# Optimization experiments

Measured on AMD Instinct MI355X. Metric: run time of the kernel, lower is better.

## Reference

```python
import jax, jax.numpy as jnp
import numpy as np

B, N, H, L, K, R = 1024, 64, 128, 4, 16, 20
CUTOFF = 5.0
GAMMA = 10.0   # RBF width
N_TYPES = 10

def _rn(k, shape, scale):
    return jax.random.normal(k, shape, jnp.float32) * scale

def setup_inputs():
    key = jax.random.key(0)
    ks = jax.random.split(key, 16)
    z = lambda *s: jnp.zeros(s, jnp.float32)
    return {
        "positions": _rn(ks[0], (B, N, 3), 2.0),
        "atomic_numbers": jax.random.randint(ks[1], (B, N), 0, N_TYPES),
        "atom_embed": _rn(ks[2], (N_TYPES, H // 4), 0.1),
        "pos_W": _rn(ks[3], (3, 3 * H // 4), 0.5),
        "pos_b": z(3 * H // 4),
        "msg_W": _rn(ks[4], (L, 2 * H + R, H), (2 * H + R) ** -0.5),
        "msg_b": z(L, H),
        "upd_W": _rn(ks[5], (L, H, H), H ** -0.5),
        "upd_b": z(L, H),
        "gself_W": _rn(ks[6], (L, H, H), H ** -0.5),
        "gmean_W": _rn(ks[7], (L, H, H), H ** -0.5),
        "g_b": z(L, H),
        "fus_W": _rn(ks[8], (L, 2 * H, H), (2 * H) ** -0.5),
        "fus_b": z(L, H),
        "ln_g": jnp.ones((L, H), jnp.float32),
        "ln_b": z(L, H),
        "cb_W1": _rn(ks[9], (L, H, 4 * H), H ** -0.5),
        "cb_b1": z(L, 4 * H),
        "cb_W2": _rn(ks[10], (L, 4 * H, H), (4 * H) ** -0.5),
        "cb_b2": z(L, H),
        "fo_W1": _rn(ks[11], (H, H), H ** -0.5),
        "fo_b1": z(H),
        "fo_W2": _rn(ks[12], (H, 3), H ** -0.5),
        "fo_b2": z(3),
    }

def _ln(x, g, b):
    m = x.mean(-1, keepdims=True)
    v = ((x - m) ** 2).mean(-1, keepdims=True)
    return (x - m) * jax.lax.rsqrt(v + 1e-5) * g + b

def reference(positions, atomic_numbers, atom_embed, pos_W, pos_b, msg_W, msg_b,
              upd_W, upd_b, gself_W, gmean_W, g_b, fus_W, fus_b, ln_g, ln_b,
              cb_W1, cb_b1, cb_W2, cb_b2, fo_W1, fo_b1, fo_W2, fo_b2):
    silu = jax.nn.silu
    Bb, Nn, _ = positions.shape
    # embeddings: atom type (H/4) || position (3H/4)
    h = jnp.concatenate([atom_embed[atomic_numbers], positions @ pos_W + pos_b], -1)  # [B,N,H]
    # kNN graph from positions (static across layers since positions are fixed)
    diff = positions[:, :, None, :] - positions[:, None, :, :]
    d2 = jnp.sum(diff * diff, -1) + jnp.eye(Nn, dtype=positions.dtype) * 1e9  # exclude self
    neg_d2, idx = jax.lax.top_k(-d2, K)                       # [B,N,K]
    d = jnp.sqrt(jnp.maximum(-neg_d2, 1e-12))
    centers = jnp.linspace(0.0, CUTOFF, R).astype(positions.dtype)
    rbf = jnp.exp(-GAMMA * (d[..., None] - centers) ** 2)     # [B,N,K,R]
    env = (0.5 * (jnp.cos(jnp.pi * d / CUTOFF) + 1.0) * (d < CUTOFF))[..., None]  # cosine cutoff
    idx_flat = idx.reshape(Bb, Nn * K)
    for i in range(msg_W.shape[0]):
        # local MPNN: gather neighbors, message MLP on [h_i, h_j, rbf], envelope, sum
        h_j = jnp.take_along_axis(h, idx_flat[:, :, None], axis=1).reshape(Bb, Nn, K, -1)
        h_i = jnp.broadcast_to(h[:, :, None, :], h_j.shape)
        m = silu(jnp.concatenate([h_i, h_j, rbf], -1) @ msg_W[i] + msg_b[i]) * env
        local = h + silu(m.sum(2) @ upd_W[i] + upd_b[i])
        # Clifford mean-field: self transform + global-mean transform
        glob = silu(h @ gself_W[i] + h.mean(1, keepdims=True) @ gmean_W[i] + g_b[i])
        # fusion (dropout is identity at inference)
        fused = silu(jnp.concatenate([local, glob], -1) @ fus_W[i] + fus_b[i])
        # Clifford block: pre-LN residual MLP
        x = _ln(fused, ln_g[i], ln_b[i])
        h = fused + silu(x @ cb_W1[i] + cb_b1[i]) @ cb_W2[i] + cb_b2[i]
    return silu(h @ fo_W1 + fo_b1) @ fo_W2 + fo_b2  # [B,N,3] forces
```

## Files before the change

kernel.cpp:

```cpp
#include <hip/hip_runtime.h>

typedef unsigned short ushort_t;
typedef unsigned int uint_t;
typedef unsigned long long ull_t;
typedef __attribute__((ext_vector_type(8))) short short8;
typedef __attribute__((ext_vector_type(4))) float f32x4;

#define B_ 1024
#define N_ 64
#define H_ 128
#define NT 256

#define IMG_WI 0
#define IMG_WJ 16384
#define IMG_UW 32768
#define IMG_GS 49152
#define IMG_FT 65536
#define IMG_FB 81920
#define IMG_C1 98304
#define IMG_C2 163840
#define IMG_GMT 229376
#define IMG_RW 245760
#define IMG_L 249856
#define IMG_FO 999424
#define WS_WEIGHTS (2u*1024u*1024u)
#define KNN_STRIDE 12288u

__device__ __forceinline__ ushort_t f2bf(float f) {
    uint_t u = __float_as_uint(f);
    return (ushort_t)((u + 0x7fffu + ((u >> 16) & 1u)) >> 16);
}
__device__ __forceinline__ float bf2f(ushort_t u) {
    union { uint_t i; float f; } v; v.i = ((uint_t)u) << 16; return v.f;
}
__device__ __forceinline__ float siluf(float x) { return x / (1.0f + __expf(-x)); }

__device__ __forceinline__ int sidx(int m, int k) {
    return m * H_ + (((k >> 3) ^ (m & 7)) << 3) + (k & 7);
}
__device__ __forceinline__ int fragoff(int m, int ch) {
    return m * H_ + ((ch ^ (m & 7)) << 3);
}

extern "C" __global__ __launch_bounds__(256)
void convert_weights(const float* __restrict__ msg_W, const float* __restrict__ upd_W,
                     const float* __restrict__ gself_W, const float* __restrict__ fus_W,
                     const float* __restrict__ cb_W1, const float* __restrict__ cb_W2,
                     const float* __restrict__ gmean_W, const float* __restrict__ fo_W1,
                     ushort_t* __restrict__ wimg)
{
    const int g = blockIdx.x;
    if (g >= 244) {
        int st = g - 244;
        ushort_t* dst = wimg + IMG_FO + st * 4096;
        for (int e = 0; e < 16; ++e) {
            int q = threadIdx.x * 16 + e;
            int n = q >> 7, k = q & 127;
            dst[q] = f2bf(fo_W1[(size_t)k * 128 + st * 32 + n]);
        }
        return;
    }
    const int l = g / 61, r = g - l * 61;
    ushort_t* base = wimg + l * IMG_L;
    if (r == 60) {
        const float* W = msg_W + l * 35328 + 256 * 128;
        ushort_t* dst = base + IMG_RW;
        for (int e = 0; e < 16; ++e) {
            int q = threadIdx.x * 16 + e;
            int sub = q >> 10, n = (q >> 5) & 31, k = q & 31;
            dst[q] = f2bf(k < 20 ? W[(size_t)k * 128 + sub * 32 + n] : 0.0f);
        }
        return;
    }
    const float* W; int ld = 128, k0 = 0, c0, off, st;
    if      (r < 4)  { W = msg_W + l * 35328;            st = r;      off = IMG_WI;  c0 = st * 32; }
    else if (r < 8)  { W = msg_W + l * 35328;  k0 = 128; st = r - 4;  off = IMG_WJ;  c0 = st * 32; }
    else if (r < 12) { W = upd_W + l * 16384;            st = r - 8;  off = IMG_UW;  c0 = st * 32; }
    else if (r < 16) { W = gself_W + l * 16384;          st = r - 12; off = IMG_GS;  c0 = st * 32; }
    else if (r < 20) { W = fus_W + l * 32768;            st = r - 16; off = IMG_FT;  c0 = st * 32; }
    else if (r < 24) { W = fus_W + l * 32768;  k0 = 128; st = r - 20; off = IMG_FB;  c0 = st * 32; }
    else if (r < 40) { W = cb_W1 + l * 65536;  ld = 512; st = r - 24; off = IMG_C1;  c0 = st * 32; }
    else if (r < 56) { int j = (r - 40) >> 2; W = cb_W2 + l * 65536; k0 = j * 128;
                       st = r - 40; off = IMG_C2; c0 = ((r - 40) & 3) * 32; }
    else             { W = gmean_W + l * 16384;          st = r - 56; off = IMG_GMT; c0 = st * 32; }
    ushort_t* dst = base + off + st * 4096;
    for (int e = 0; e < 16; ++e) {
        int q = threadIdx.x * 16 + e;
        int n = q >> 7, k = q & 127;
        dst[q] = f2bf(W[(size_t)(k0 + k) * ld + c0 + n]);
    }
}

extern "C" __global__ __launch_bounds__(64)
void knn_kernel(const float* __restrict__ positions, char* __restrict__ ws)
{
    const int b = blockIdx.x, lane = threadIdx.x;
    float px = positions[b * 192 + lane * 3 + 0];
    float py = positions[b * 192 + lane * 3 + 1];
    float pz = positions[b * 192 + lane * 3 + 2];
    float* kd = (float*)(ws + WS_WEIGHTS + (size_t)b * KNN_STRIDE);
    float* ke = kd + 1024;
    ushort_t* ki = (ushort_t*)(ke + 1024);
    for (int n = 0; n < 64; ++n) {
        float dx = __fsub_rn(__shfl(px, n), px);
        float dy = __fsub_rn(__shfl(py, n), py);
        float dz = __fsub_rn(__shfl(pz, n), pz);
        float d2 = __fadd_rn(__fadd_rn(__fmul_rn(dx, dx), __fmul_rn(dy, dy)), __fmul_rn(dz, dz));
        if (lane == n) d2 = 1e30f;
        float sd = 0.f; int si = 0;
        for (int k = 0; k < 16; ++k) {
            float dmin = d2;
            #pragma unroll
            for (int o = 1; o < 64; o <<= 1) dmin = fminf(dmin, __shfl_xor(dmin, o));
            ull_t mask = __ballot(d2 == dmin);
            int widx = __ffsll(mask) - 1;
            if (lane == widx) d2 = 1e30f;
            if (lane == k) { si = widx; sd = dmin; }
        }
        if (lane < 16) {
            float dd = sqrtf(fmaxf(sd, 1e-12f));
            kd[n * 16 + lane] = dd;
            ke[n * 16 + lane] = (dd < 5.0f) ? 0.5f * (__cosf(0.62831853071795864769f * dd) + 1.0f) : 0.0f;
            ki[n * 16 + lane] = (ushort_t)si;
        }
    }
}

#define HFS 132
struct __align__(16) Smem {
    ushort_t T1[N_ * H_];
    ushort_t T2[N_ * H_];
    float Hf[N_ * HFS];
    float d[1024];
    float env[1024];
    ushort_t idx[1024];
    char u[2048];
};

__device__ __forceinline__ f32x4 gemm_s(const short8 a[4], const ushort_t* __restrict__ img,
                                        int s, int l15, int quad)
{
    const ushort_t* base = img + ((s >> 1) << 12) + ((((s & 1) << 4) + l15) << 7) + quad * 8;
    short8 b0 = *(const short8*)(base);
    short8 b1 = *(const short8*)(base + 32);
    short8 b2 = *(const short8*)(base + 64);
    short8 b3 = *(const short8*)(base + 96);
    f32x4 c = {0.f, 0.f, 0.f, 0.f};
    c = __builtin_amdgcn_mfma_f32_16x16x32_bf16(a[0], b0, c, 0, 0, 0);
    c = __builtin_amdgcn_mfma_f32_16x16x32_bf16(a[1], b1, c, 0, 0, 0);
    c = __builtin_amdgcn_mfma_f32_16x16x32_bf16(a[2], b2, c, 0, 0, 0);
    c = __builtin_amdgcn_mfma_f32_16x16x32_bf16(a[3], b3, c, 0, 0, 0);
    return c;
}
__device__ __forceinline__ f32x4 gemm_s_acc(const short8 a[4], const ushort_t* __restrict__ img,
                                            int s, int l15, int quad, f32x4 c)
{
    const ushort_t* base = img + ((s >> 1) << 12) + ((((s & 1) << 4) + l15) << 7) + quad * 8;
    short8 b0 = *(const short8*)(base);
    short8 b1 = *(const short8*)(base + 32);
    short8 b2 = *(const short8*)(base + 64);
    short8 b3 = *(const short8*)(base + 96);
    c = __builtin_amdgcn_mfma_f32_16x16x32_bf16(a[0], b0, c, 0, 0, 0);
    c = __builtin_amdgcn_mfma_f32_16x16x32_bf16(a[1], b1, c, 0, 0, 0);
    c = __builtin_amdgcn_mfma_f32_16x16x32_bf16(a[2], b2, c, 0, 0, 0);
    c = __builtin_amdgcn_mfma_f32_16x16x32_bf16(a[3], b3, c, 0, 0, 0);
    return c;
}
__device__ __forceinline__ void loadA(const ushort_t* __restrict__ X, int mrow, int quad, short8 a[4]) {
    #pragma unroll
    for (int kc = 0; kc < 4; ++kc) a[kc] = *(const short8*)&X[fragoff(mrow, kc * 4 + quad)];
}
__device__ __forceinline__ void buildA(const float* __restrict__ Hf, int mrow, int quad, short8 a[4]) {
    #pragma unroll
    for (int kc = 0; kc < 4; ++kc) {
        const float* p = Hf + mrow * HFS + (kc * 4 + quad) * 8;
        float4 u0 = *(const float4*)p;
        float4 u1 = *(const float4*)(p + 4);
        short8 v;
        v[0] = (short)f2bf(u0.x); v[1] = (short)f2bf(u0.y);
        v[2] = (short)f2bf(u0.z); v[3] = (short)f2bf(u0.w);
        v[4] = (short)f2bf(u1.x); v[5] = (short)f2bf(u1.y);
        v[6] = (short)f2bf(u1.z); v[7] = (short)f2bf(u1.w);
        a[kc] = v;
    }
}

extern "C" __global__ __launch_bounds__(NT, 2)
void md17_fused_kernel(
    const float* __restrict__ positions, const int* __restrict__ atomic_numbers,
    const float* __restrict__ atom_embed, const float* __restrict__ pos_W,
    const float* __restrict__ pos_b,
    const float* __restrict__ msg_b, const float* __restrict__ upd_b,
    const float* __restrict__ g_b, const float* __restrict__ fus_b,
    const float* __restrict__ ln_g, const float* __restrict__ ln_b,
    const float* __restrict__ cb_b1, const float* __restrict__ cb_b2,
    const float* __restrict__ fo_b1,
    const float* __restrict__ fo_W2, const float* __restrict__ fo_b2,
    char* __restrict__ ws, float* __restrict__ out)
{
    __shared__ Smem sm;
    const int b = blockIdx.x;
    const int tid = threadIdx.x;
    const int wave = tid >> 6, lane = tid & 63;
    const int quad = lane >> 4, l15 = lane & 15;
    const int mrow = wave * 16 + l15;
    const int rbase = wave * 16 + quad * 4;

    const ushort_t* wimg = (const ushort_t*)ws;
    float* spos = (float*)sm.u;
    ushort_t* part = (ushort_t*)sm.u;
    float* hmean = (float*)(sm.u + 1024);
    float* gvec  = (float*)(sm.u + 1536);

    {
        const char* kb = ws + WS_WEIGHTS + (size_t)b * KNN_STRIDE;
        const float* kd = (const float*)kb;
        const float* ke = (const float*)(kb + 4096);
        const uint_t* ki = (const uint_t*)(kb + 8192);
        for (int t = tid; t < 1024; t += NT) { sm.d[t] = kd[t]; sm.env[t] = ke[t]; }
        for (int t = tid; t < 512; t += NT) ((uint_t*)sm.idx)[t] = ki[t];
        if (tid < 192) spos[tid] = positions[b * 192 + tid];
    }
    __syncthreads();
    for (int t = tid; t < N_ * H_; t += NT) {
        int n = t >> 7, f = t & 127;
        float v;
        if (f < 32) {
            v = atom_embed[atomic_numbers[b * N_ + n] * 32 + f];
        } else {
            int j = f - 32;
            v = pos_b[j];
            #pragma unroll
            for (int c = 0; c < 3; ++c)
                v = fmaf(spos[n * 3 + c], pos_W[c * 96 + j], v);
        }
        sm.Hf[n * HFS + f] = v;
        sm.T1[sidx(n, f)] = f2bf(v);
    }
    __syncthreads();

    #pragma unroll 1
    for (int l = 0; l < 4; ++l) {
        const ushort_t* wl = wimg + l * IMG_L;
        const float* mb  = msg_b + l * H_;
        const float* ub  = upd_b + l * H_;
        const float* gb  = g_b + l * H_;
        const float* fb  = fus_b + l * H_;
        const float* lg  = ln_g + l * H_;
        const float* lb  = ln_b + l * H_;
        const float* c1b = cb_b1 + l * 4 * H_;
        const float* c2b = cb_b2 + l * H_;

        #pragma unroll
        for (int s = 0; s < 8; ++s) {
            int col = s * 16 + l15;
            const float* hp = sm.Hf + rbase * HFS + col;
            float p = hp[0] + hp[HFS] + hp[2 * HFS] + hp[3 * HFS];
            p += __shfl_xor(p, 16);
            p += __shfl_xor(p, 32);
            if (quad == 0) part[wave * 128 + col] = f2bf(p);
        }
        __syncthreads();
        if (tid < H_)
            hmean[tid] = (bf2f(part[tid]) + bf2f(part[128 + tid])
                        + bf2f(part[256 + tid]) + bf2f(part[384 + tid])) * (1.0f / 64.0f);
        __syncthreads();

        if (tid < H_) {
            float s = gb[tid];
            const ushort_t* wrow = wl + IMG_GMT + tid * 128;
            for (int c = 0; c < 128; c += 8) {
                short8 w = *(const short8*)(wrow + c);
                #pragma unroll
                for (int i = 0; i < 8; ++i) s = fmaf(hmean[c + i], bf2f((ushort_t)w[i]), s);
            }
            gvec[tid] = s;
        }
        {
            short8 a_h[4]; loadA(sm.T1, mrow, quad, a_h);
            #pragma unroll
            for (int s = 0; s < 8; ++s) {
                f32x4 c = gemm_s(a_h, wl + IMG_WI, s, l15, quad);
                int col = s * 16 + l15; float bv = mb[col];
                #pragma unroll
                for (int r = 0; r < 4; ++r)
                    sm.T1[sidx(rbase + r, col)] = f2bf(c[r] + bv);
            }
            #pragma unroll
            for (int s = 0; s < 8; ++s) {
                f32x4 c = gemm_s(a_h, wl + IMG_WJ, s, l15, quad);
                int col = s * 16 + l15;
                #pragma unroll
                for (int r = 0; r < 4; ++r)
                    sm.T2[sidx(rbase + r, col)] = f2bf(c[r]);
            }
        }
        __syncthreads();

        {
            float ccv[8];
            #pragma unroll
            for (int j = 0; j < 8; ++j)
                ccv[j] = (float)((double)(quad * 8 + j) * (5.0 / 19.0));
            #pragma unroll 1
            for (int g = 0; g < 16; ++g) {
                int n = wave * 16 + g;
                int jv[4]; float ev[4];
                #pragma unroll
                for (int r = 0; r < 4; ++r) {
                    int k = quad * 4 + r;
                    jv[r] = sm.idx[n * 16 + k];
                    ev[r] = sm.env[n * 16 + k];
                }
                float ddm = sm.d[n * 16 + l15];
                short8 arb;
                #pragma unroll
                for (int j = 0; j < 8; ++j) {
                    float t2 = ddm - ccv[j];
                    float rv = __expf(-10.0f * t2 * t2);
                    arb[j] = (short)((quad * 8 + j) < 20 ? f2bf(rv) : (ushort_t)0);
                }
                #pragma unroll
                for (int s = 0; s < 8; ++s) {
                    int col = s * 16 + l15;
                    const ushort_t* rbase_p = wl + IMG_RW + ((s >> 1) << 10)
                                            + ((((s & 1) << 4) + l15) << 5) + quad * 8;
                    short8 brw = *(const short8*)rbase_p;
                    f32x4 c = {0.f, 0.f, 0.f, 0.f};
                    c = __builtin_amdgcn_mfma_f32_16x16x32_bf16(arb, brw, c, 0, 0, 0);
                    float ai = bf2f(sm.T1[sidx(n, col)]);
                    float acc = 0.f;
                    #pragma unroll
                    for (int r = 0; r < 4; ++r) {
                        float gm = bf2f(sm.T2[sidx(jv[r], col)]);
                        acc = fmaf(siluf(ai + gm + c[r]), ev[r], acc);
                    }
                    acc += __shfl_xor(acc, 16);
                    acc += __shfl_xor(acc, 32);
                    if (quad == 0) sm.T1[sidx(n, col)] = f2bf(acc);
                }
            }
        }
        __syncthreads();


        {
            short8 a_m[4]; loadA(sm.T1, mrow, quad, a_m);
            #pragma unroll
            for (int s = 0; s < 8; ++s) {
                f32x4 c = gemm_s(a_m, wl + IMG_UW, s, l15, quad);
                int col = s * 16 + l15; float bv = ub[col];
                #pragma unroll
                for (int r = 0; r < 4; ++r)
                    sm.T2[sidx(rbase + r, col)] = f2bf(sm.Hf[(rbase + r) * HFS + col] + siluf(c[r] + bv));
            }
            short8 a_hh[4]; buildA(sm.Hf, mrow, quad, a_hh);
            #pragma unroll
            for (int s = 0; s < 8; ++s) {
                f32x4 c = gemm_s(a_hh, wl + IMG_GS, s, l15, quad);
                int col = s * 16 + l15; float gv = gvec[col];
                #pragma unroll
                for (int r = 0; r < 4; ++r)
                    sm.T1[sidx(rbase + r, col)] = f2bf(siluf(c[r] + gv));
            }
        }

        float sr[4] = {0.f, 0.f, 0.f, 0.f}, qr[4] = {0.f, 0.f, 0.f, 0.f};
        {
            short8 a_t[4];
            loadA(sm.T2, mrow, quad, a_t);
            #pragma unroll
            for (int s = 0; s < 8; ++s) {
                f32x4 c = gemm_s(a_t, wl + IMG_FT, s, l15, quad);
                int col = s * 16 + l15;
                int rb = rbase * HFS + col;
                sm.Hf[rb] = c[0]; sm.Hf[rb + HFS] = c[1];
                sm.Hf[rb + 2 * HFS] = c[2]; sm.Hf[rb + 3 * HFS] = c[3];
            }
            loadA(sm.T1, mrow, quad, a_t);
            #pragma unroll
            for (int s = 0; s < 8; ++s) {
                f32x4 c = gemm_s(a_t, wl + IMG_FB, s, l15, quad);
                int col = s * 16 + l15; float bv = fb[col];
                int rb = rbase * HFS + col;
                #pragma unroll
                for (int r = 0; r < 4; ++r) {
                    float v = siluf(sm.Hf[rb + r * HFS] + c[r] + bv);
                    sm.Hf[rb + r * HFS] = v;
                    sr[r] += v; qr[r] += v * v;
                }
            }
            #pragma unroll
            for (int o = 1; o < 16; o <<= 1) {
                #pragma unroll
                for (int r = 0; r < 4; ++r) {
                    sr[r] += __shfl_xor(sr[r], o);
                    qr[r] += __shfl_xor(qr[r], o);
                }
            }
        }

        #pragma unroll
        for (int r = 0; r < 4; ++r) {
            float mu = sr[r] * (1.0f / 128.0f);
            float var = qr[r] * (1.0f / 128.0f) - mu * mu;
            float rs = rsqrtf(var + 1e-5f);
            int row = rbase + r;
            #pragma unroll
            for (int s = 0; s < 8; ++s) {
                int col = s * 16 + l15;
                sm.T1[sidx(row, col)] = f2bf((sm.Hf[row * HFS + col] - mu) * rs * lg[col] + lb[col]);
            }
        }

        {
            short8 a_x[4]; loadA(sm.T1, mrow, quad, a_x);
            f32x4 acc2[8];
            #pragma unroll
            for (int s = 0; s < 8; ++s) acc2[s] = (f32x4){0.f, 0.f, 0.f, 0.f};
            #pragma unroll 1
            for (int j = 0; j < 4; ++j) {
                #pragma unroll
                for (int s = 0; s < 8; ++s) {
                    f32x4 c = gemm_s(a_x, wl + IMG_C1 + j * 16384, s, l15, quad);
                    int col = s * 16 + l15; float bv = c1b[j * H_ + col];
                    #pragma unroll
                    for (int r = 0; r < 4; ++r)
                        sm.T2[sidx(rbase + r, col)] = f2bf(siluf(c[r] + bv));
                }
                short8 a_t[4]; loadA(sm.T2, mrow, quad, a_t);
                #pragma unroll
                for (int s = 0; s < 8; ++s)
                    acc2[s] = gemm_s_acc(a_t, wl + IMG_C2 + j * 16384, s, l15, quad, acc2[s]);
            }
            #pragma unroll
            for (int s = 0; s < 8; ++s) {
                int col = s * 16 + l15; float bv = c2b[col];
                #pragma unroll
                for (int r = 0; r < 4; ++r) {
                    int row = rbase + r;
                    float v = sm.Hf[row * HFS + col] + acc2[s][r] + bv;
                    sm.Hf[row * HFS + col] = v;
                    sm.T1[sidx(row, col)] = f2bf(v);
                }
            }
        }
    }

    {
        short8 a_f[4]; loadA(sm.T1, mrow, quad, a_f);
        #pragma unroll
        for (int s = 0; s < 8; ++s) {
            f32x4 c = gemm_s(a_f, wimg + IMG_FO, s, l15, quad);
            int col = s * 16 + l15; float bv = fo_b1[col];
            #pragma unroll
            for (int r = 0; r < 4; ++r)
                sm.T2[sidx(rbase + r, col)] = f2bf(siluf(c[r] + bv));
        }
    }
    __syncthreads();
    if (tid < 192) {
        int n = tid / 3, j = tid - n * 3;
        float s = fo_b2[j];
        for (int c = 0; c < H_; ++c)
            s = fmaf(bf2f(sm.T2[sidx(n, c)]), fo_W2[c * 3 + j], s);
        out[b * 192 + tid] = s;
    }
}

extern "C" void kernel_launch(void* const* d_in, const int* in_sizes, int n_in,
                              void* d_out, int out_size, void* d_ws, size_t ws_size,
                              hipStream_t stream) {
    (void)in_sizes; (void)n_in; (void)out_size; (void)ws_size;
    convert_weights<<<248, 256, 0, stream>>>(
        (const float*)d_in[5], (const float*)d_in[7], (const float*)d_in[9],
        (const float*)d_in[12], (const float*)d_in[16], (const float*)d_in[18],
        (const float*)d_in[10], (const float*)d_in[20], (ushort_t*)d_ws);
    knn_kernel<<<B_, 64, 0, stream>>>((const float*)d_in[0], (char*)d_ws);
    md17_fused_kernel<<<B_, NT, 0, stream>>>(
        (const float*)d_in[0], (const int*)d_in[1],
        (const float*)d_in[2], (const float*)d_in[3], (const float*)d_in[4],
        (const float*)d_in[6], (const float*)d_in[8],
        (const float*)d_in[11], (const float*)d_in[13],
        (const float*)d_in[14], (const float*)d_in[15],
        (const float*)d_in[17], (const float*)d_in[19],
        (const float*)d_in[21],
        (const float*)d_in[22], (const float*)d_in[23],
        (char*)d_ws, (float*)d_out);
}
```

Measured before the change: 1.484 ms.

## Keep fp32 residual state in registers instead of shared memory; allow three blocks per CU

The fp32 hidden state per row/column, previously held in a padded shared-memory array, now lives in per-thread registers laid out to match the MFMA output fragment. All residual adds, LayerNorm statistics, the mean reduction and the gself GEMM input now read it from registers or from the existing bf16 copy. This removes about 33 KB of LDS per block and many LDS reads and writes, and raises the launch-bounds minimum to 3 blocks per CU. The trade-off is 32 extra live registers per thread under a tighter register budget, which risks spilling. With 1024 blocks the higher occupancy may not shorten the tail.

```diff
diff --git a/kernel.cpp b/kernel.cpp
--- a/kernel.cpp
+++ b/kernel.cpp
@@ -126,11 +126,9 @@
     }
 }
 
-#define HFS 132
 struct __align__(16) Smem {
     ushort_t T1[N_ * H_];
     ushort_t T2[N_ * H_];
-    float Hf[N_ * HFS];
     float d[1024];
     float env[1024];
     ushort_t idx[1024];
@@ -170,22 +168,8 @@
     #pragma unroll
     for (int kc = 0; kc < 4; ++kc) a[kc] = *(const short8*)&X[fragoff(mrow, kc * 4 + quad)];
 }
-__device__ __forceinline__ void buildA(const float* __restrict__ Hf, int mrow, int quad, short8 a[4]) {
-    #pragma unroll
-    for (int kc = 0; kc < 4; ++kc) {
-        const float* p = Hf + mrow * HFS + (kc * 4 + quad) * 8;
-        float4 u0 = *(const float4*)p;
-        float4 u1 = *(const float4*)(p + 4);
-        short8 v;
-        v[0] = (short)f2bf(u0.x); v[1] = (short)f2bf(u0.y);
-        v[2] = (short)f2bf(u0.z); v[3] = (short)f2bf(u0.w);
-        v[4] = (short)f2bf(u1.x); v[5] = (short)f2bf(u1.y);
-        v[6] = (short)f2bf(u1.z); v[7] = (short)f2bf(u1.w);
-        a[kc] = v;
-    }
-}
-
-extern "C" __global__ __launch_bounds__(NT, 2)
+
+extern "C" __global__ __launch_bounds__(NT, 3)
 void md17_fused_kernel(
     const float* __restrict__ positions, const int* __restrict__ atomic_numbers,
     const float* __restrict__ atom_embed, const float* __restrict__ pos_W,
@@ -212,6 +196,8 @@
     float* hmean = (float*)(sm.u + 1024);
     float* gvec  = (float*)(sm.u + 1536);
 
+    float hreg[8][4];
+
     {
         const char* kb = ws + WS_WEIGHTS + (size_t)b * KNN_STRIDE;
         const float* kd = (const float*)kb;
@@ -222,20 +208,29 @@
         if (tid < 192) spos[tid] = positions[b * 192 + tid];
     }
     __syncthreads();
-    for (int t = tid; t < N_ * H_; t += NT) {
-        int n = t >> 7, f = t & 127;
-        float v;
-        if (f < 32) {
-            v = atom_embed[atomic_numbers[b * N_ + n] * 32 + f];
-        } else {
-            int j = f - 32;
-            v = pos_b[j];
-            #pragma unroll
-            for (int c = 0; c < 3; ++c)
-                v = fmaf(spos[n * 3 + c], pos_W[c * 96 + j], v);
-        }
-        sm.Hf[n * HFS + f] = v;
-        sm.T1[sidx(n, f)] = f2bf(v);
+    {
+        int an[4];
+        #pragma unroll
+        for (int r = 0; r < 4; ++r) an[r] = atomic_numbers[b * N_ + rbase + r];
+        #pragma unroll
+        for (int s = 0; s < 8; ++s) {
+            int col = s * 16 + l15;
+            #pragma unroll
+            for (int r = 0; r < 4; ++r) {
+                float v;
+                if (s < 2) {
+                    v = atom_embed[an[r] * 32 + col];
+                } else {
+                    int j = col - 32;
+                    v = pos_b[j];
+                    #pragma unroll
+                    for (int c = 0; c < 3; ++c)
+                        v = fmaf(spos[(rbase + r) * 3 + c], pos_W[c * 96 + j], v);
+                }
+                hreg[s][r] = v;
+                sm.T1[sidx(rbase + r, col)] = f2bf(v);
+            }
+        }
     }
     __syncthreads();
 
@@ -254,8 +249,7 @@
         #pragma unroll
         for (int s = 0; s < 8; ++s) {
             int col = s * 16 + l15;
-            const float* hp = sm.Hf + rbase * HFS + col;
-            float p = hp[0] + hp[HFS] + hp[2 * HFS] + hp[3 * HFS];
+            float p = hreg[s][0] + hreg[s][1] + hreg[s][2] + hreg[s][3];
             p += __shfl_xor(p, 16);
             p += __shfl_xor(p, 32);
             if (quad == 0) part[wave * 128 + col] = f2bf(p);
@@ -266,6 +260,7 @@
                         + bf2f(part[256 + tid]) + bf2f(part[384 + tid])) * (1.0f / 64.0f);
         __syncthreads();
 
+        short8 a_h[4];
         if (tid < H_) {
             float s = gb[tid];
             const ushort_t* wrow = wl + IMG_GMT + tid * 128;
@@ -277,7 +272,7 @@
             gvec[tid] = s;
         }
         {
-            short8 a_h[4]; loadA(sm.T1, mrow, quad, a_h);
+            loadA(sm.T1, mrow, quad, a_h);
             #pragma unroll
             for (int s = 0; s < 8; ++s) {
                 f32x4 c = gemm_s(a_h, wl + IMG_WI, s, l15, quad);
@@ -352,12 +347,11 @@
                 int col = s * 16 + l15; float bv = ub[col];
                 #pragma unroll
                 for (int r = 0; r < 4; ++r)
-                    sm.T2[sidx(rbase + r, col)] = f2bf(sm.Hf[(rbase + r) * HFS + col] + siluf(c[r] + bv));
-            }
-            short8 a_hh[4]; buildA(sm.Hf, mrow, quad, a_hh);
-            #pragma unroll
-            for (int s = 0; s < 8; ++s) {
-                f32x4 c = gemm_s(a_hh, wl + IMG_GS, s, l15, quad);
+                    sm.T2[sidx(rbase + r, col)] = f2bf(hreg[s][r] + siluf(c[r] + bv));
+            }
+            #pragma unroll
+            for (int s = 0; s < 8; ++s) {
+                f32x4 c = gemm_s(a_h, wl + IMG_GS, s, l15, quad);
                 int col = s * 16 + l15; float gv = gvec[col];
                 #pragma unroll
                 for (int r = 0; r < 4; ++r)
@@ -372,21 +366,18 @@
             #pragma unroll
             for (int s = 0; s < 8; ++s) {
                 f32x4 c = gemm_s(a_t, wl + IMG_FT, s, l15, quad);
-                int col = s * 16 + l15;
-                int rb = rbase * HFS + col;
-                sm.Hf[rb] = c[0]; sm.Hf[rb + HFS] = c[1];
-                sm.Hf[rb + 2 * HFS] = c[2]; sm.Hf[rb + 3 * HFS] = c[3];
+                #pragma unroll
+                for (int r = 0; r < 4; ++r) hreg[s][r] = c[r];
             }
             loadA(sm.T1, mrow, quad, a_t);
             #pragma unroll
             for (int s = 0; s < 8; ++s) {
                 f32x4 c = gemm_s(a_t, wl + IMG_FB, s, l15, quad);
                 int col = s * 16 + l15; float bv = fb[col];
-                int rb = rbase * HFS + col;
                 #pragma unroll
                 for (int r = 0; r < 4; ++r) {
-                    float v = siluf(sm.Hf[rb + r * HFS] + c[r] + bv);
-                    sm.Hf[rb + r * HFS] = v;
+                    float v = siluf(hreg[s][r] + c[r] + bv);
+                    hreg[s][r] = v;
                     sr[r] += v; qr[r] += v * v;
                 }
             }
@@ -409,7 +400,7 @@
             #pragma unroll
             for (int s = 0; s < 8; ++s) {
                 int col = s * 16 + l15;
-                sm.T1[sidx(row, col)] = f2bf((sm.Hf[row * HFS + col] - mu) * rs * lg[col] + lb[col]);
+                sm.T1[sidx(row, col)] = f2bf((hreg[s][r] - mu) * rs * lg[col] + lb[col]);
             }
         }
 
@@ -438,10 +429,9 @@
                 int col = s * 16 + l15; float bv = c2b[col];
                 #pragma unroll
                 for (int r = 0; r < 4; ++r) {
-                    int row = rbase + r;
-                    float v = sm.Hf[row * HFS + col] + acc2[s][r] + bv;
-                    sm.Hf[row * HFS + col] = v;
-                    sm.T1[sidx(row, col)] = f2bf(v);
+                    float v = hreg[s][r] + acc2[s][r] + bv;
+                    hreg[s][r] = v;
+                    sm.T1[sidx(rbase + r, col)] = f2bf(v);
                 }
             }
         }
```

After: 1.664 ms. 1.12x slower.
